# Optimization experiments

Measured on AMD Instinct MI355X. Metric: run time of the kernel, lower is better.

Reference implementation:

```python
import jax, jax.numpy as jnp
import numpy as np

N = 100000          # nodes
E = 1600000         # edges (avg degree 16)
D_IN = 128          # in_features
D_OUT = 128         # out_features


def setup_inputs() -> dict:
    key = jax.random.key(0)
    k1, k2, k3, k4 = jax.random.split(key, 4)
    H = jax.random.normal(k1, (N, D_IN), dtype=jnp.float32)
    # COO indices of sparse adjacency A: row i aggregates features of col j
    src = jax.random.randint(k2, (E,), 0, N, dtype=jnp.int32)
    dst = jax.random.randint(k3, (E,), 0, N, dtype=jnp.int32)
    # nn.Linear(2*in_features, out_features): weight [out, 2*in], zero bias
    W = jax.random.normal(k4, (D_OUT, 2 * D_IN), dtype=jnp.float32) * 0.05
    b = jnp.zeros((D_OUT,), dtype=jnp.float32)
    return {"H": H, "src": src, "dst": dst, "W": W, "b": b}


def reference(H, src, dst, W, b):
    # max-aggregation: for each node i, max over features of its neighbors.
    # One fused gather + segment-max replaces the per-node Python loop.
    gathered = H[dst]  # [E, D_IN]
    agg = jax.ops.segment_max(gathered, src, num_segments=N)  # [N, D_IN]
    # nodes with no incoming edges stay zero (torch code leaves zeros)
    deg = jax.ops.segment_sum(jnp.ones((src.shape[0],), jnp.float32), src,
                              num_segments=N)  # [N]
    H_neigh = jnp.where(deg[:, None] > 0, agg, 0.0)
    H_concat = jnp.concatenate([H, H_neigh], axis=1)  # [N, 2*D_IN]
    return H_concat @ W.T + b
```

## Files before the change

kernel.cpp:

```cpp
#include <hip/hip_runtime.h>
#include <math.h>

#define NN 100000
#define NE 1600000
#define DD 128
#define NBINS 3125
#define CAP 640
#define PB 196
#define CB 196

#define WS_HH  0
#define WS_CUR 6400000
#define WS_ENT (WS_CUR + NBINS)
#define WS_AH  (WS_ENT + NBINS * CAP)
#define WS_WH  (WS_AH + NN * (DD / 2))

typedef __attribute__((ext_vector_type(8))) _Float16 h8_t;
typedef __attribute__((ext_vector_type(4))) _Float16 h4_t;
typedef __attribute__((ext_vector_type(2))) _Float16 h2_t;
typedef __attribute__((ext_vector_type(4))) float f4_t;

__device__ __forceinline__ unsigned pk2h(float x, float y) {
    h2_t h;
    h.x = (_Float16)x;
    h.y = (_Float16)y;
    return *(unsigned*)&h;
}

__device__ __forceinline__ h4_t h4max(h4_t a, h4_t b) {
    return __builtin_elementwise_max(a, b);
}

__global__ __launch_bounds__(1024) void prep_kernel(const float* __restrict__ H,
                                                    const int* __restrict__ src,
                                                    const int* __restrict__ dst,
                                                    int* __restrict__ cursor,
                                                    unsigned* __restrict__ entries,
                                                    uint4* __restrict__ Hh4,
                                                    const float* __restrict__ W,
                                                    unsigned* __restrict__ Wh) {
    __shared__ int cnt[NBINS];
    __shared__ int gcur[NBINS];
    const int t = threadIdx.x;
    const int b = blockIdx.x;
    if (b < PB) {
        for (int i = t; i < NBINS; i += 1024) cnt[i] = 0;
        __syncthreads();
        const int base = b * 8192;
        int sv[8];
#pragma unroll
        for (int k = 0; k < 8; ++k) {
            int e = base + k * 1024 + t;
            sv[k] = (e < NE) ? src[e] : -1;
            if (sv[k] >= 0) atomicAdd(&cnt[sv[k] >> 5], 1);
        }
        __syncthreads();
        for (int i = t; i < NBINS; i += 1024) {
            int c = cnt[i];
            gcur[i] = c ? i * CAP + atomicAdd(&cursor[i], c) : 0;
        }
        __syncthreads();
#pragma unroll
        for (int k = 0; k < 8; ++k) {
            int e = base + k * 1024 + t;
            if (sv[k] >= 0) {
                int s = sv[k];
                int pos = atomicAdd(&gcur[s >> 5], 1);
                entries[pos] = ((unsigned)(s & 31) << 17) | (unsigned)dst[e];
            }
        }
    } else if (b < PB + CB) {
        const int nb = b - PB;
        const int n8 = NN * DD / 8;
        for (int i = nb * 1024 + t; i < n8; i += CB * 1024) {
            const float4* s = (const float4*)H + (size_t)i * 2;
            float4 a = s[0], c4 = s[1];
            uint4 o;
            o.x = pk2h(a.x, a.y);
            o.y = pk2h(a.z, a.w);
            o.z = pk2h(c4.x, c4.y);
            o.w = pk2h(c4.z, c4.w);
            Hh4[i] = o;
        }
    } else {
        for (int i = t; i < 128 * 256 / 2; i += 1024)
            Wh[i] = pk2h(W[2 * i], W[2 * i + 1]);
    }
}

__global__ __launch_bounds__(256) void agg_kernel(const _Float16* __restrict__ Hh,
                                                  const int* __restrict__ cursor,
                                                  const unsigned* __restrict__ entries,
                                                  unsigned* __restrict__ Ah) {
    __shared__ unsigned raw[CAP];
    __shared__ unsigned sorted[CAP];
    __shared__ int cnt[32], base_s[32], cur[32];
    const int t = threadIdx.x;
    const int b = blockIdx.x;
    const int n = cursor[b];

    if (t < 32) cnt[t] = 0;
    __syncthreads();
    for (int i = t; i < n; i += 256) {
        unsigned e = entries[b * CAP + i];
        raw[i] = e;
        atomicAdd(&cnt[e >> 17], 1);
    }
    __syncthreads();
    if (t < 32) {
        int v = cnt[t];
        int incl = v;
#pragma unroll
        for (int o = 1; o < 32; o <<= 1) {
            int y = __shfl_up(incl, o, 32);
            if (t >= o) incl += y;
        }
        base_s[t] = incl - v;
        cur[t] = incl - v;
    }
    __syncthreads();
    for (int i = t; i < n; i += 256) {
        unsigned e = raw[i];
        int pos = atomicAdd(&cur[e >> 17], 1);
        sorted[pos] = e & 0x1FFFFu;
    }
    __syncthreads();

    const int lane = t & 63;
    const int w = t >> 6;
    const int half = lane >> 5;
    const int l32 = lane & 31;
    const _Float16* __restrict__ colbase = Hh + l32 * 4;
#pragma unroll
    for (int q = 0; q < 8; ++q) {
        int ln = w * 8 + q;
        int s0 = base_s[ln];
        int e0 = s0 + cnt[ln];
        unsigned long long mu = 0xFC00FC00FC00FC00ull;
        h4_t m = *(h4_t*)&mu;
        int j = s0 + half;
        for (; j + 6 < e0; j += 8) {
            int d0 = sorted[j], d1 = sorted[j + 2];
            int d2 = sorted[j + 4], d3 = sorted[j + 6];
            h4_t v0 = *(const h4_t*)(colbase + (size_t)d0 * DD);
            h4_t v1 = *(const h4_t*)(colbase + (size_t)d1 * DD);
            h4_t v2 = *(const h4_t*)(colbase + (size_t)d2 * DD);
            h4_t v3 = *(const h4_t*)(colbase + (size_t)d3 * DD);
            m = h4max(m, h4max(h4max(v0, v1), h4max(v2, v3)));
        }
        for (; j < e0; j += 2) {
            h4_t v0 = *(const h4_t*)(colbase + (size_t)sorted[j] * DD);
            m = h4max(m, v0);
        }
        uint2 mv = *(uint2*)&m;
        uint2 ov;
        ov.x = (unsigned)__shfl_xor((int)mv.x, 32, 64);
        ov.y = (unsigned)__shfl_xor((int)mv.y, 32, 64);
        h4_t om = *(h4_t*)&ov;
        m = h4max(m, om);
        int node = b * 32 + ln;
        if (half == 0 && node < NN) {
            uint2 outv = make_uint2(0u, 0u);
            if (s0 < e0) outv = *(uint2*)&m;
            *(uint2*)(Ah + (size_t)node * 64 + l32 * 2) = outv;
        }
    }
}

__global__ __launch_bounds__(256) void mfma_matmul_kernel(
        const unsigned short* __restrict__ Hh,
        const unsigned short* __restrict__ Ah,
        const unsigned short* __restrict__ Wh,
        const float* __restrict__ bias,
        float* __restrict__ out) {
    const int t = threadIdx.x;
    const int lane = t & 63;
    const int w = t >> 6;
    const int quad = lane >> 4;
    const int l16 = lane & 15;
    const int arow = blockIdx.x * 64 + w * 16 + l16;
    const bool aok = arow < NN;

    f4_t acc[8] = {};
#pragma unroll
    for (int c = 0; c < 4; ++c) {
        const unsigned short* xb = (c < 2) ? Hh : Ah;
        const int koff = (c & 1) * 64;
#pragma unroll
        for (int kk = 0; kk < 64; kk += 32) {
            uint4 av = make_uint4(0, 0, 0, 0);
            if (aok)
                av = *(const uint4*)(xb + (size_t)arow * DD + koff + kk + quad * 8);
            h8_t a = *(h8_t*)&av;
#pragma unroll
            for (int ot = 0; ot < 8; ++ot) {
                h8_t bf = *(const h8_t*)(Wh + (size_t)(ot * 16 + l16) * 256
                                         + c * 64 + kk + quad * 8);
                acc[ot] = __builtin_amdgcn_mfma_f32_16x16x32_f16(a, bf, acc[ot], 0, 0, 0);
            }
        }
    }

#pragma unroll
    for (int ot = 0; ot < 8; ++ot) {
        float bv = bias[ot * 16 + l16];
#pragma unroll
        for (int reg = 0; reg < 4; ++reg) {
            int row = blockIdx.x * 64 + w * 16 + quad * 4 + reg;
            if (row < NN)
                out[(size_t)row * DD + ot * 16 + l16] = acc[ot][reg] + bv;
        }
    }
}

extern "C" void kernel_launch(void* const* d_in, const int* in_sizes, int n_in,
                              void* d_out, int out_size, void* d_ws, size_t ws_size,
                              hipStream_t stream) {
    const float* H   = (const float*)d_in[0];
    const int*   src = (const int*)d_in[1];
    const int*   dst = (const int*)d_in[2];
    const float* W   = (const float*)d_in[3];
    const float* b   = (const float*)d_in[4];
    float* out = (float*)d_out;

    int* ws = (int*)d_ws;
    unsigned short* Hh      = (unsigned short*)(ws + WS_HH);
    int*            cursor  = ws + WS_CUR;
    unsigned*       entries = (unsigned*)(ws + WS_ENT);
    unsigned*       Ah      = (unsigned*)(ws + WS_AH);
    unsigned*       Wh      = (unsigned*)(ws + WS_WH);

    hipMemsetAsync(cursor, 0, NBINS * sizeof(int), stream);
    prep_kernel<<<PB + CB + 1, 1024, 0, stream>>>(H, src, dst, cursor, entries,
                                                  (uint4*)Hh, W, Wh);
    agg_kernel<<<NBINS, 256, 0, stream>>>((const _Float16*)Hh, cursor, entries, Ah);
    mfma_matmul_kernel<<<(NN + 63) / 64, 256, 0, stream>>>(
        Hh, (const unsigned short*)Ah, (const unsigned short*)Wh, b, out);
}
```

Measured before the change: 264.0 us.

## Stage X and W tiles in LDS for matmul and double rows per wave

The matmul kernel now loads 128-row activation tiles and weight tiles into padded shared memory, and each wave computes 32 rows with two accumulator sets. Weight fragments are reused across two MFMA row blocks instead of being re-read from global memory for every 16 rows. The fp16 conversion blocks in the prep kernel are also doubled. This costs extra LDS, barriers and more accumulator registers, and launches fewer matmul blocks.

```diff
diff --git a/kernel.cpp b/kernel.cpp
--- a/kernel.cpp
+++ b/kernel.cpp
@@ -7,7 +7,7 @@
 #define NBINS 3125
 #define CAP 640
 #define PB 196
-#define CB 196
+#define CB 392
 
 #define WS_HH  0
 #define WS_CUR 6400000
@@ -167,48 +167,75 @@
     }
 }
 
+#define XP 72
 __global__ __launch_bounds__(256) void mfma_matmul_kernel(
         const unsigned short* __restrict__ Hh,
         const unsigned short* __restrict__ Ah,
         const unsigned short* __restrict__ Wh,
         const float* __restrict__ bias,
         float* __restrict__ out) {
+    __shared__ unsigned short Xs[128 * XP];
+    __shared__ unsigned short Ws[128 * XP];
     const int t = threadIdx.x;
     const int lane = t & 63;
     const int w = t >> 6;
     const int quad = lane >> 4;
     const int l16 = lane & 15;
-    const int arow = blockIdx.x * 64 + w * 16 + l16;
-    const bool aok = arow < NN;
-
-    f4_t acc[8] = {};
-#pragma unroll
+    const int blockrow = blockIdx.x * 128;
+
+    f4_t acc[2][8] = {};
+
     for (int c = 0; c < 4; ++c) {
-        const unsigned short* xb = (c < 2) ? Hh : Ah;
-        const int koff = (c & 1) * 64;
+        const int k0 = c * 64;
+        {
+            const unsigned short* xb = (c < 2) ? Hh : Ah;
+            const int koff = (c < 2) ? k0 : k0 - 128;
+            const int seg = t & 7, r0 = t >> 3;
+#pragma unroll
+            for (int j = 0; j < 4; ++j) {
+                int r = r0 + 32 * j;
+                int row = blockrow + r;
+                uint4 v = make_uint4(0, 0, 0, 0);
+                if (row < NN)
+                    v = *(const uint4*)(xb + (size_t)row * DD + koff + seg * 8);
+                *(uint4*)&Xs[r * XP + seg * 8] = v;
+            }
+        }
+        {
+            const int seg = t & 7, o0 = t >> 3;
+#pragma unroll
+            for (int j = 0; j < 4; ++j) {
+                int o = o0 + 32 * j;
+                uint4 v = *(const uint4*)(Wh + (size_t)o * 256 + k0 + seg * 8);
+                *(uint4*)&Ws[o * XP + seg * 8] = v;
+            }
+        }
+        __syncthreads();
 #pragma unroll
         for (int kk = 0; kk < 64; kk += 32) {
-            uint4 av = make_uint4(0, 0, 0, 0);
-            if (aok)
-                av = *(const uint4*)(xb + (size_t)arow * DD + koff + kk + quad * 8);
-            h8_t a = *(h8_t*)&av;
+            h8_t a0 = *(const h8_t*)&Xs[(w * 32 + l16) * XP + kk + quad * 8];
+            h8_t a1 = *(const h8_t*)&Xs[(w * 32 + 16 + l16) * XP + kk + quad * 8];
 #pragma unroll
             for (int ot = 0; ot < 8; ++ot) {
-                h8_t bf = *(const h8_t*)(Wh + (size_t)(ot * 16 + l16) * 256
-                                         + c * 64 + kk + quad * 8);
-                acc[ot] = __builtin_amdgcn_mfma_f32_16x16x32_f16(a, bf, acc[ot], 0, 0, 0);
-            }
-        }
+                h8_t bf = *(const h8_t*)&Ws[(ot * 16 + l16) * XP + kk + quad * 8];
+                acc[0][ot] = __builtin_amdgcn_mfma_f32_16x16x32_f16(a0, bf, acc[0][ot], 0, 0, 0);
+                acc[1][ot] = __builtin_amdgcn_mfma_f32_16x16x32_f16(a1, bf, acc[1][ot], 0, 0, 0);
+            }
+        }
+        __syncthreads();
     }
 
 #pragma unroll
     for (int ot = 0; ot < 8; ++ot) {
         float bv = bias[ot * 16 + l16];
 #pragma unroll
-        for (int reg = 0; reg < 4; ++reg) {
-            int row = blockIdx.x * 64 + w * 16 + quad * 4 + reg;
-            if (row < NN)
-                out[(size_t)row * DD + ot * 16 + l16] = acc[ot][reg] + bv;
+        for (int sub = 0; sub < 2; ++sub) {
+#pragma unroll
+            for (int reg = 0; reg < 4; ++reg) {
+                int row = blockrow + w * 32 + sub * 16 + quad * 4 + reg;
+                if (row < NN)
+                    out[(size_t)row * DD + ot * 16 + l16] = acc[sub][ot][reg] + bv;
+            }
         }
     }
 }
@@ -234,6 +261,6 @@
     prep_kernel<<<PB + CB + 1, 1024, 0, stream>>>(H, src, dst, cursor, entries,
                                                   (uint4*)Hh, W, Wh);
     agg_kernel<<<NBINS, 256, 0, stream>>>((const _Float16*)Hh, cursor, entries, Ah);
-    mfma_matmul_kernel<<<(NN + 63) / 64, 256, 0, stream>>>(
+    mfma_matmul_kernel<<<(NN + 127) / 128, 256, 0, stream>>>(
         Hh, (const unsigned short*)Ah, (const unsigned short*)Wh, b, out);
 }
```

New measurement: 244.0 us. 1.08x faster.
